# Kernel tuning notes

Hardware: AMD Instinct MI355X
Metric: run time of the kernel (lower is better)

The kernel has to match this reference:

```python
import jax, jax.numpy as jnp
import numpy as np

N, E = 50000, 800000
IN, HID, OUT = 128, 32, 8


def setup_inputs() -> dict:
    key = jax.random.key(0)
    ks = jax.random.split(key, 20)
    f32 = jnp.float32
    def rn(k, shape, s=0.1):
        return (jax.random.normal(k, shape, dtype=f32) * s)
    return {
        'x': jax.random.normal(ks[0], (N, IN), dtype=f32),
        'edge_index': jax.random.randint(ks[1], (2, E), 0, N, dtype=jnp.int32),
        'edge_attr': jax.random.uniform(ks[2], (E, 1), dtype=f32),
        # layer 1: heads=4, out=HID, concat -> 4*HID channels
        'w1l': rn(ks[3], (IN, 4 * HID)), 'b1l': rn(ks[4], (4 * HID,)),
        'w1r': rn(ks[5], (IN, 4 * HID)), 'b1r': rn(ks[6], (4 * HID,)),
        'w1e': rn(ks[7], (1, 4 * HID)),
        'att1': rn(ks[8], (4, HID)), 'bias1': rn(ks[9], (4 * HID,)),
        # layer 2: heads=2, out=HID, mean over heads -> HID channels
        'w2l': rn(ks[10], (4 * HID, 2 * HID)), 'b2l': rn(ks[11], (2 * HID,)),
        'w2r': rn(ks[12], (4 * HID, 2 * HID)), 'b2r': rn(ks[13], (2 * HID,)),
        'w2e': rn(ks[14], (1, 2 * HID)),
        'att2': rn(ks[15], (2, HID)), 'bias2': rn(ks[16], (HID,)),
        'wc': rn(ks[17], (HID, OUT)), 'bc': rn(ks[18], (OUT,)),
    }


def _add_self_loops(edge_index, edge_attr, n):
    # PyG GATv2Conv adds self-loops; edge feature for loops = mean of edge_attr
    loop = jnp.arange(n, dtype=edge_index.dtype)
    src = jnp.concatenate([edge_index[0], loop])
    dst = jnp.concatenate([edge_index[1], loop])
    mean_attr = jnp.broadcast_to(edge_attr.mean(axis=0), (n, edge_attr.shape[1]))
    ea = jnp.concatenate([edge_attr, mean_attr], axis=0)
    return src, dst, ea


def _gatv2(x, src, dst, eattr, Wl, bl, Wr, br, We, att, bias, heads, out, concat):
    n = x.shape[0]
    xl = (x @ Wl + bl).reshape(n, heads, out)   # source transform (messages)
    xr = (x @ Wr + br).reshape(n, heads, out)   # target transform
    e = (eattr @ We).reshape(-1, heads, out)    # edge embedding
    z = jax.nn.leaky_relu(xl[src] + xr[dst] + e, negative_slope=0.2)  # [Etot,H,D]
    score = jnp.einsum('ehd,hd->eh', z, att)
    # segment softmax over incoming edges of each destination node
    smax = jax.ops.segment_max(score, dst, num_segments=n)
    ex = jnp.exp(score - smax[dst])
    denom = jax.ops.segment_sum(ex, dst, num_segments=n)
    alpha = ex / denom[dst]                     # [Etot,H]
    agg = jax.ops.segment_sum(xl[src] * alpha[..., None], dst, num_segments=n)
    o = agg.reshape(n, heads * out) if concat else agg.mean(axis=1)
    return o + bias


def reference(x, edge_index, edge_attr, w1l, b1l, w1r, b1r, w1e, att1, bias1,
              w2l, b2l, w2r, b2r, w2e, att2, bias2, wc, bc):
    src, dst, ea = _add_self_loops(edge_index, edge_attr, x.shape[0])
    h = _gatv2(x, src, dst, ea, w1l, b1l, w1r, b1r, w1e, att1, bias1, 4, HID, True)
    h = jax.nn.elu(h)
    # dropout p=0.4 is training-only; reference is eval mode (identity)
    h = _gatv2(h, src, dst, ea, w2l, b2l, w2r, b2r, w2e, att2, bias2, 2, HID, False)
    h = jax.nn.elu(h)
    return h @ wc + bc
```

## Files before the change

kernel.cpp:

```cpp
#include <hip/hip_runtime.h>
#include <hip/hip_fp16.h>
#include <math.h>

typedef _Float16 h2_t __attribute__((ext_vector_type(2)));
typedef _Float16 h4_t __attribute__((ext_vector_type(4)));
typedef _Float16 h8_t __attribute__((ext_vector_type(8)));
typedef float f4_t __attribute__((ext_vector_type(4)));
typedef float f8_t __attribute__((ext_vector_type(8)));

#define PRE_BLOCKS 512

__device__ inline h8_t load8f_to_h8(const float* p) {
    float4 a = *(const float4*)p;
    float4 b = *(const float4*)(p + 4);
    h8_t r;
    r[0] = (_Float16)a.x; r[1] = (_Float16)a.y; r[2] = (_Float16)a.z; r[3] = (_Float16)a.w;
    r[4] = (_Float16)b.x; r[5] = (_Float16)b.y; r[6] = (_Float16)b.z; r[7] = (_Float16)b.w;
    return r;
}

__device__ inline h4_t load4f_to_h4(const float* p) {
    float4 a = *(const float4*)p;
    h4_t r;
    r[0] = (_Float16)a.x; r[1] = (_Float16)a.y; r[2] = (_Float16)a.z; r[3] = (_Float16)a.w;
    return r;
}

__device__ inline float dot8h(h8_t a, h8_t b, float s) {
    s = __builtin_amdgcn_fdot2(__builtin_shufflevector(a, a, 0, 1),
                               __builtin_shufflevector(b, b, 0, 1), s, false);
    s = __builtin_amdgcn_fdot2(__builtin_shufflevector(a, a, 2, 3),
                               __builtin_shufflevector(b, b, 2, 3), s, false);
    s = __builtin_amdgcn_fdot2(__builtin_shufflevector(a, a, 4, 5),
                               __builtin_shufflevector(b, b, 4, 5), s, false);
    s = __builtin_amdgcn_fdot2(__builtin_shufflevector(a, a, 6, 7),
                               __builtin_shufflevector(b, b, 6, 7), s, false);
    return s;
}

__device__ inline float dot4h(h4_t a, h4_t b, float s) {
    s = __builtin_amdgcn_fdot2(__builtin_shufflevector(a, a, 0, 1),
                               __builtin_shufflevector(b, b, 0, 1), s, false);
    s = __builtin_amdgcn_fdot2(__builtin_shufflevector(a, a, 2, 3),
                               __builtin_shufflevector(b, b, 2, 3), s, false);
    return s;
}

__device__ inline float elu1(float v) { return v > 0.f ? v : __expf(v) - 1.f; }

struct MA {
    const float* x;
    const float* eattr;
    const int* ei;
    const float *w1l, *b1l, *w1r, *b1r, *w1e, *att1, *bias1;
    const float *w2l, *b2l, *w2r, *b2r, *w2e, *att2, *bias2;
    const float *wc, *bc;
    float* out;
    _Float16 *xh, *xl1h, *xr1h, *h1h, *xl2h, *xr2h;
    _Float16 *p1l, *p1r, *p2l, *p2r;
    int *cnt, *offb, *rank;
    unsigned* flags;
    float* part;
    unsigned* edges;
    int N, E, NBs, NW;
    float invE;
};


__device__ inline void phase_packw(const MA& a, int g) {
    const float* W;
    _Float16* P;
    int M, lg;
    if (g < 2048)      { W = a.w1l; P = a.p1l; M = 128; lg = g; }
    else if (g < 4096) { W = a.w1r; P = a.p1r; M = 128; lg = g - 2048; }
    else if (g < 5120) { W = a.w2l; P = a.p2l; M = 64;  lg = g - 4096; }
    else               { W = a.w2r; P = a.p2r; M = 64;  lg = g - 5120; }
    int ln = lg & 63;
    int s = (lg >> 6) & 3;
    int tt = lg >> 8;
    int m = ln & 15, quad = ln >> 4;
    h8_t v;
#pragma unroll
    for (int j = 0; j < 8; ++j)
        v[j] = (_Float16)W[(size_t)(s * 32 + quad * 8 + j) * M + tt * 16 + m];
    *(h8_t*)(P + (size_t)lg * 8) = v;
}

template <int NT>
__device__ inline void phase_mm_tile(const MA& a, const _Float16* X, int rt, int lane,
                                     const _Float16* Pl, const float* bl, _Float16* Yl,
                                     const _Float16* Pr, const float* br, _Float16* Yr) {
    int nrow = lane & 15, quad = lane >> 4;
    int row = rt * 16 + nrow;
    if (row >= a.N) return;
    const _Float16* xp = X + (size_t)row * 128 + quad * 8;
    h8_t bf0 = *(const h8_t*)(xp);
    h8_t bf1 = *(const h8_t*)(xp + 32);
    h8_t bf2 = *(const h8_t*)(xp + 64);
    h8_t bf3 = *(const h8_t*)(xp + 96);
#pragma unroll
    for (int w = 0; w < 2; ++w) {
        const _Float16* P = w ? Pr : Pl;
        const float* bias = w ? br : bl;
        _Float16* Y = w ? Yr : Yl;
#pragma unroll
        for (int t2 = 0; t2 < NT; ++t2) {
            f4_t acc = {0.f, 0.f, 0.f, 0.f};
            const _Float16* pb = P + (size_t)t2 * 2048 + (size_t)lane * 8;
            acc = __builtin_amdgcn_mfma_f32_16x16x32_f16(*(const h8_t*)pb, bf0, acc, 0, 0, 0);
            acc = __builtin_amdgcn_mfma_f32_16x16x32_f16(*(const h8_t*)(pb + 512), bf1, acc, 0, 0, 0);
            acc = __builtin_amdgcn_mfma_f32_16x16x32_f16(*(const h8_t*)(pb + 1024), bf2, acc, 0, 0, 0);
            acc = __builtin_amdgcn_mfma_f32_16x16x32_f16(*(const h8_t*)(pb + 1536), bf3, acc, 0, 0, 0);
            float4 bv = *(const float4*)(bias + t2 * 16 + quad * 4);
            h4_t o;
            o[0] = (_Float16)(acc[0] + bv.x);
            o[1] = (_Float16)(acc[1] + bv.y);
            o[2] = (_Float16)(acc[2] + bv.z);
            o[3] = (_Float16)(acc[3] + bv.w);
            *(h4_t*)(Y + (size_t)row * (NT * 16) + t2 * 16 + quad * 4) = o;
        }
    }
}


__global__ __launch_bounds__(256) void k_pre(MA a) {
    if (blockIdx.x >= PRE_BLOCKS) {
        int g = (blockIdx.x - PRE_BLOCKS) * 256 + threadIdx.x;
        if (g < 6144) phase_packw(a, g);
        return;
    }
    int t = blockIdx.x * 256 + threadIdx.x;
    const int stride = PRE_BLOCKS * 256;
    for (int i = t; i < a.N; i += stride) a.cnt[i] = 0;
    for (int i = t; i < a.NBs; i += stride) a.flags[i] = 0u;
    int nchunk = (a.N * 128) >> 3;
    for (int i = t; i < nchunk; i += stride) {
        h8_t v = load8f_to_h8(a.x + (size_t)i * 8);
        *(h8_t*)(a.xh + (size_t)i * 8) = v;
    }
    float s = 0.f;
    for (int i = t; i < a.E; i += stride) s += a.eattr[i];
    __shared__ float sd[4];
    for (int o = 1; o < 64; o <<= 1) s += __shfl_xor(s, o, 64);
    if ((threadIdx.x & 63) == 0) sd[threadIdx.x >> 6] = s;
    __syncthreads();
    if (threadIdx.x == 0) a.part[blockIdx.x] = sd[0] + sd[1] + sd[2] + sd[3];
}


#define CNT_BLOCKS 1600

__global__ __launch_bounds__(256) void k_mmcnt(MA a) {
    int bid = blockIdx.x;
    if (bid < a.NW) {
        int wid = bid * 4 + (threadIdx.x >> 6);
        int ntile = (a.N + 15) / 16;
        if (wid < ntile)
            phase_mm_tile<8>(a, a.xh, wid, threadIdx.x & 63,
                             a.p1l, a.b1l, a.xl1h, a.p1r, a.b1r, a.xr1h);
    } else {
        int t = (bid - a.NW) * 256 + threadIdx.x;
        const int stride = CNT_BLOCKS * 256;
        for (int e = t; e < a.E; e += stride)
            a.rank[e] = atomicAdd(&a.cnt[a.ei[a.E + e]], 1);
    }
}


__global__ __launch_bounds__(256, 1) void k_scan(MA a) {
    __shared__ int tmp[256];
    __shared__ int sbase;
    __shared__ float smean;
    int tx = threadIdx.x;
    int b = blockIdx.x;
    int i = b * 256 + tx;
    {
        float s = a.part[tx] + a.part[tx + 256];
        for (int o = 1; o < 64; o <<= 1) s += __shfl_xor(s, o, 64);
        __shared__ float sd[4];
        if ((tx & 63) == 0) sd[tx >> 6] = s;
        __syncthreads();
        if (tx == 0) smean = (sd[0] + sd[1] + sd[2] + sd[3]) * a.invE;
    }
    int v = (i < a.N) ? a.cnt[i] + 1 : 0;
    tmp[tx] = v;
    __syncthreads();
    for (int o = 1; o < 256; o <<= 1) {
        int tv = (tx >= o) ? tmp[tx - o] : 0;
        __syncthreads();
        tmp[tx] += tv;
        __syncthreads();
    }
    int T = tmp[255];
    if (tx == 0) {
        if (b == 0) {
            atomicExch(&a.flags[0], (2u << 30) | (unsigned)T);
            sbase = 0;
        } else {
            atomicExch(&a.flags[b], (1u << 30) | (unsigned)T);
            int running = 0;
            int j = b - 1;
            while (true) {
                unsigned f = atomicAdd(&a.flags[j], 0u);
                unsigned st = f >> 30;
                if (st == 0u) continue;
                running += (int)(f & 0x3FFFFFFFu);
                if (st == 2u) break;
                --j;
            }
            atomicExch(&a.flags[b], (2u << 30) | (unsigned)(running + T));
            sbase = running;
        }
    }
    __syncthreads();
    if (i < a.N) {
        int o = sbase + tmp[tx] - v;
        a.offb[i] = o;
        unsigned qv = (unsigned)__float2int_rn(smean * 255.f);
        a.edges[o] = (unsigned)i | (qv << 24);
    }
}


__global__ __launch_bounds__(256) void k_fill(MA a) {
    int e = blockIdx.x * 256 + threadIdx.x;
    if (e >= a.E) return;
    int d = a.ei[a.E + e];
    int pos = a.offb[d] + 1 + a.rank[e];
    unsigned qv = (unsigned)__float2int_rn(a.eattr[e] * 255.f);
    a.edges[pos] = (unsigned)a.ei[e] | (qv << 24);
}


__global__ __launch_bounds__(256) void k_node1(MA a) {
    int lane = threadIdx.x & 63;
    int node = blockIdx.x * 4 + (threadIdx.x >> 6);
    if (node >= a.N) return;
    int g = lane >> 4;
    int q = lane & 15;
    int c0 = q * 8;

    h8_t xrv = *(const h8_t*)(a.xr1h + (size_t)node * 128 + c0);
    h8_t wev = load8f_to_h8(a.w1e + c0);
    h8_t atv = load8f_to_h8(a.att1 + c0);
    int start = a.offb[node];
    int deg1 = a.cnt[node] + 1;
    int last = deg1 - 1;

    float l = 0.f;
    f8_t acc = {0.f, 0.f, 0.f, 0.f, 0.f, 0.f, 0.f, 0.f};
    for (int i = 0; i < deg1; i += 16) {
        int s0 = i + g, s1 = i + 4 + g, s2 = i + 8 + g, s3 = i + 12 + g;
        unsigned p0 = a.edges[start + min(s0, last)];
        unsigned p1 = a.edges[start + min(s1, last)];
        unsigned p2 = a.edges[start + min(s2, last)];
        unsigned p3 = a.edges[start + min(s3, last)];
        h8_t x0 = *(const h8_t*)(a.xl1h + (size_t)(p0 & 0x00FFFFFFu) * 128 + c0);
        h8_t x1 = *(const h8_t*)(a.xl1h + (size_t)(p1 & 0x00FFFFFFu) * 128 + c0);
        h8_t x2 = *(const h8_t*)(a.xl1h + (size_t)(p2 & 0x00FFFFFFu) * 128 + c0);
        h8_t x3 = *(const h8_t*)(a.xl1h + (size_t)(p3 & 0x00FFFFFFu) * 128 + c0);
        float e0 = (float)(p0 >> 24) * (1.f / 255.f);
        float e1 = (float)(p1 >> 24) * (1.f / 255.f);
        float e2 = (float)(p2 >> 24) * (1.f / 255.f);
        float e3 = (float)(p3 >> 24) * (1.f / 255.f);
        h8_t z0 = x0 + xrv + wev * (_Float16)e0;
        z0 = __builtin_elementwise_max(z0, z0 * (_Float16)0.2f);
        float sc0 = dot8h(z0, atv, 0.f);
        h8_t z1 = x1 + xrv + wev * (_Float16)e1;
        z1 = __builtin_elementwise_max(z1, z1 * (_Float16)0.2f);
        float sc1 = dot8h(z1, atv, 0.f);
        h8_t z2 = x2 + xrv + wev * (_Float16)e2;
        z2 = __builtin_elementwise_max(z2, z2 * (_Float16)0.2f);
        float sc2 = dot8h(z2, atv, 0.f);
        h8_t z3 = x3 + xrv + wev * (_Float16)e3;
        z3 = __builtin_elementwise_max(z3, z3 * (_Float16)0.2f);
        float sc3 = dot8h(z3, atv, 0.f);
        sc0 += __shfl_xor(sc0, 1, 64); sc0 += __shfl_xor(sc0, 2, 64);
        sc1 += __shfl_xor(sc1, 1, 64); sc1 += __shfl_xor(sc1, 2, 64);
        sc2 += __shfl_xor(sc2, 1, 64); sc2 += __shfl_xor(sc2, 2, 64);
        sc3 += __shfl_xor(sc3, 1, 64); sc3 += __shfl_xor(sc3, 2, 64);
        float pA = (s0 < deg1) ? __expf(fminf(sc0, 60.f)) : 0.f;
        float pB = (s1 < deg1) ? __expf(fminf(sc1, 60.f)) : 0.f;
        float pC = (s2 < deg1) ? __expf(fminf(sc2, 60.f)) : 0.f;
        float pD = (s3 < deg1) ? __expf(fminf(sc3, 60.f)) : 0.f;
        l += (pA + pB) + (pC + pD);
#pragma unroll
        for (int k = 0; k < 8; ++k)
            acc[k] = fmaf(pA, (float)x0[k],
                     fmaf(pB, (float)x1[k],
                     fmaf(pC, (float)x2[k], fmaf(pD, (float)x3[k], acc[k]))));
    }
#pragma unroll
    for (int k = 0; k < 8; ++k) {
        acc[k] += __shfl_xor(acc[k], 16, 64);
        acc[k] += __shfl_xor(acc[k], 32, 64);
    }
    l += __shfl_xor(l, 16, 64);
    l += __shfl_xor(l, 32, 64);
    if (g == 0) {
        float inv = 1.f / l;
        float4 b0 = *(const float4*)(a.bias1 + c0);
        float4 b1 = *(const float4*)(a.bias1 + c0 + 4);
        float bb[8] = {b0.x, b0.y, b0.z, b0.w, b1.x, b1.y, b1.z, b1.w};
        h8_t o;
#pragma unroll
        for (int k = 0; k < 8; ++k) o[k] = (_Float16)elu1(fmaf(acc[k], inv, bb[k]));
        *(h8_t*)(a.h1h + (size_t)node * 128 + c0) = o;
    }
}


__global__ __launch_bounds__(256) void k_mm4(MA a) {
    int wid = blockIdx.x * 4 + (threadIdx.x >> 6);
    int ntile = (a.N + 15) / 16;
    if (wid >= ntile) return;
    phase_mm_tile<4>(a, a.h1h, wid, threadIdx.x & 63,
                     a.p2l, a.b2l, a.xl2h, a.p2r, a.b2r, a.xr2h);
}


__global__ __launch_bounds__(256) void k_node2(MA a) {
    __shared__ float h2s[16][33];
    int tid = threadIdx.x;
    int lane = tid & 63;
    int wib = tid >> 6;
    int sub = lane >> 4;
    int r = lane & 15;
    int nloc = wib * 4 + sub;
    int node = blockIdx.x * 16 + nloc;
    int c0 = r * 4;

    if (node < a.N) {
        h4_t xrv = *(const h4_t*)(a.xr2h + (size_t)node * 64 + c0);
        h4_t wev = load4f_to_h4(a.w2e + c0);
        h4_t atv = load4f_to_h4(a.att2 + c0);
        int start = a.offb[node];
        int deg1 = a.cnt[node] + 1;
        int last = deg1 - 1;
        float l = 0.f;
        float acc[4] = {0.f, 0.f, 0.f, 0.f};
        for (int i = 0; i < deg1; i += 4) {
            unsigned p[4];
            h4_t xv[4];
#pragma unroll
            for (int j = 0; j < 4; ++j) p[j] = a.edges[start + min(i + j, last)];
#pragma unroll
            for (int j = 0; j < 4; ++j)
                xv[j] = *(const h4_t*)(a.xl2h + (size_t)(p[j] & 0x00FFFFFFu) * 64 + c0);
#pragma unroll
            for (int j = 0; j < 4; ++j) {
                float ea = (float)(p[j] >> 24) * (1.f / 255.f);
                h4_t z = xv[j] + xrv + wev * (_Float16)ea;
                z = __builtin_elementwise_max(z, z * (_Float16)0.2f);
                float sc = dot4h(z, atv, 0.f);
                sc += __shfl_xor(sc, 1, 64);
                sc += __shfl_xor(sc, 2, 64);
                sc += __shfl_xor(sc, 4, 64);
                float pp = (i + j < deg1) ? __expf(fminf(sc, 60.f)) : 0.f;
                l += pp;
#pragma unroll
                for (int k = 0; k < 4; ++k) acc[k] = fmaf(pp, (float)xv[j][k], acc[k]);
            }
        }
        float inv = 1.f / l;
#pragma unroll
        for (int k = 0; k < 4; ++k) {
            float norm = acc[k] * inv;
            float other = __shfl_xor(norm, 8, 64);
            float v = 0.5f * (norm + other);
            if (r < 8) h2s[nloc][c0 + k] = elu1(v + a.bias2[c0 + k]);
        }
    }
    __syncthreads();
    if (tid < 128) {
        int n = tid >> 3, j = tid & 7;
        int gnode = blockIdx.x * 16 + n;
        if (gnode < a.N) {
            float acc = a.bc[j];
#pragma unroll 8
            for (int d = 0; d < 32; ++d) acc = fmaf(h2s[n][d], a.wc[d * 8 + j], acc);
            a.out[(size_t)gnode * 8 + j] = acc;
        }
    }
}


extern "C" void kernel_launch(void* const* d_in, const int* in_sizes, int n_in,
                              void* d_out, int out_size, void* d_ws, size_t ws_size,
                              hipStream_t stream) {
    const int N = in_sizes[0] / 128;
    const int E = in_sizes[2];
    const int tot = E + N;

    char* ws = (char*)d_ws;
    size_t o = 0;
    auto alloc = [&](size_t bytes) -> void* {
        void* p = ws + o;
        o += (bytes + 255) & ~(size_t)255;
        return p;
    };
    MA a;
    a.x     = (const float*)d_in[0];
    a.ei    = (const int*)d_in[1];
    a.eattr = (const float*)d_in[2];
    a.w1l = (const float*)d_in[3];  a.b1l = (const float*)d_in[4];
    a.w1r = (const float*)d_in[5];  a.b1r = (const float*)d_in[6];
    a.w1e = (const float*)d_in[7];  a.att1 = (const float*)d_in[8];
    a.bias1 = (const float*)d_in[9];
    a.w2l = (const float*)d_in[10]; a.b2l = (const float*)d_in[11];
    a.w2r = (const float*)d_in[12]; a.b2r = (const float*)d_in[13];
    a.w2e = (const float*)d_in[14]; a.att2 = (const float*)d_in[15];
    a.bias2 = (const float*)d_in[16];
    a.wc = (const float*)d_in[17];  a.bc = (const float*)d_in[18];
    a.out = (float*)d_out;

    a.xh   = (_Float16*)alloc((size_t)N * 128 * 2);
    a.xl1h = (_Float16*)alloc((size_t)N * 128 * 2);
    a.xr1h = (_Float16*)alloc((size_t)N * 128 * 2);
    a.h1h  = (_Float16*)alloc((size_t)N * 128 * 2);
    a.xl2h = (_Float16*)alloc((size_t)N * 64 * 2);
    a.xr2h = (_Float16*)alloc((size_t)N * 64 * 2);
    a.p1l  = (_Float16*)alloc(128 * 128 * 2);
    a.p1r  = (_Float16*)alloc(128 * 128 * 2);
    a.p2l  = (_Float16*)alloc(128 * 64 * 2);
    a.p2r  = (_Float16*)alloc(128 * 64 * 2);
    a.cnt  = (int*)alloc((size_t)N * 4);
    a.offb = (int*)alloc((size_t)N * 4);
    a.rank = (int*)alloc((size_t)E * 4);
    a.flags = (unsigned*)alloc(1024 * 4);
    a.part  = (float*)alloc(PRE_BLOCKS * 4);
    a.edges = (unsigned*)alloc((size_t)tot * 4);
    a.N = N;
    a.E = E;
    a.NBs = (N + 255) / 256;
    a.NW = (N + 63) / 64;
    a.invE = 1.0f / (float)E;

    k_pre<<<PRE_BLOCKS + 24, 256, 0, stream>>>(a);
    k_mmcnt<<<a.NW + CNT_BLOCKS, 256, 0, stream>>>(a);
    k_scan<<<a.NBs, 256, 0, stream>>>(a);
    k_fill<<<(E + 255) / 256, 256, 0, stream>>>(a);
    k_node1<<<(N + 3) / 4, 256, 0, stream>>>(a);
    k_mm4<<<(N + 63) / 64, 256, 0, stream>>>(a);
    k_node2<<<(N + 15) / 16, 256, 0, stream>>>(a);
}
```

Baseline: 279.4 us.

## Replace global atomic CSR build with two-level bucketed counting sort

Builds the destination-sorted edge list by radix-style bucketing: per-block LDS histograms over 64-node buckets, a column scan with decoupled lookback, LDS-atomic scatter into a temporary 64-bit buffer, then a per-bucket fine sort that computes offsets and degrees. This replaces per-edge global atomics on node counters and the separate rank array and fill pass. The aim is to remove contended global atomics and random scattered writes. In exchange it adds an extra pass over an 8-byte-per-edge temp buffer and a serial lookback scan.

```diff
diff --git a/kernel.cpp b/kernel.cpp
--- a/kernel.cpp
+++ b/kernel.cpp
@@ -9,6 +9,8 @@
 typedef float f8_t __attribute__((ext_vector_type(8)));
 
 #define PRE_BLOCKS 512
+#define SB 512
+#define NBUK_PAD 800
 
 __device__ inline h8_t load8f_to_h8(const float* p) {
     float4 a = *(const float4*)p;
@@ -58,11 +60,15 @@
     float* out;
     _Float16 *xh, *xl1h, *xr1h, *h1h, *xl2h, *xr2h;
     _Float16 *p1l, *p1r, *p2l, *p2r;
-    int *cnt, *offb, *rank;
+    int *deg, *offb;
+    unsigned* parth;
+    unsigned *tstart, *tot;
+    unsigned* smeanq;
+    unsigned long long* tmp;
     unsigned* flags;
     float* part;
     unsigned* edges;
-    int N, E, NBs, NW;
+    int N, E, NW, NBK, CE;
     float invE;
 };
 
@@ -129,10 +135,14 @@
         if (g < 6144) phase_packw(a, g);
         return;
     }
-    int t = blockIdx.x * 256 + threadIdx.x;
+    __shared__ unsigned bh[NBUK_PAD];
+    __shared__ float sd[4];
+    int tx = threadIdx.x;
+    for (int j = tx; j < NBUK_PAD; j += 256) bh[j] = 0u;
+
+    int t = blockIdx.x * 256 + tx;
     const int stride = PRE_BLOCKS * 256;
-    for (int i = t; i < a.N; i += stride) a.cnt[i] = 0;
-    for (int i = t; i < a.NBs; i += stride) a.flags[i] = 0u;
+    for (int i = t; i < NBUK_PAD; i += stride) a.flags[i] = 0u;
     int nchunk = (a.N * 128) >> 3;
     for (int i = t; i < nchunk; i += stride) {
         h8_t v = load8f_to_h8(a.x + (size_t)i * 8);
@@ -140,17 +150,77 @@
     }
     float s = 0.f;
     for (int i = t; i < a.E; i += stride) s += a.eattr[i];
-    __shared__ float sd[4];
     for (int o = 1; o < 64; o <<= 1) s += __shfl_xor(s, o, 64);
-    if ((threadIdx.x & 63) == 0) sd[threadIdx.x >> 6] = s;
-    __syncthreads();
-    if (threadIdx.x == 0) a.part[blockIdx.x] = sd[0] + sd[1] + sd[2] + sd[3];
-}
-
-
-#define CNT_BLOCKS 1600
-
-__global__ __launch_bounds__(256) void k_mmcnt(MA a) {
+    if ((tx & 63) == 0) sd[tx >> 6] = s;
+    __syncthreads();
+    if (tx == 0) a.part[blockIdx.x] = sd[0] + sd[1] + sd[2] + sd[3];
+
+    int e0 = blockIdx.x * a.CE, e1 = min(e0 + a.CE, a.E);
+    for (int e = e0 + tx; e < e1; e += 256)
+        atomicAdd(&bh[((unsigned)a.ei[a.E + e]) >> 6], 1u);
+    __syncthreads();
+    for (int j = tx; j < NBUK_PAD; j += 256)
+        a.parth[(size_t)blockIdx.x * NBUK_PAD + j] = bh[j];
+}
+
+
+__global__ __launch_bounds__(512, 1) void k_colscan(MA a) {
+    __shared__ unsigned lds[512];
+    __shared__ unsigned sbase;
+    __shared__ float sd[8];
+    int tx = threadIdx.x;
+    int b = blockIdx.x;
+    unsigned v = a.parth[(size_t)tx * NBUK_PAD + b];
+    lds[tx] = v;
+    __syncthreads();
+    for (int o = 1; o < 512; o <<= 1) {
+        unsigned u = (tx >= o) ? lds[tx - o] : 0u;
+        __syncthreads();
+        lds[tx] += u;
+        __syncthreads();
+    }
+    unsigned T = lds[511];
+    unsigned excl = lds[tx] - v;
+    if (tx == 0) {
+        unsigned run = 0;
+        if (b == 0) {
+            atomicExch(&a.flags[0], (2u << 30) | T);
+        } else {
+            atomicExch(&a.flags[b], (1u << 30) | T);
+            int j = b - 1;
+            while (true) {
+                unsigned f = atomicAdd(&a.flags[j], 0u);
+                unsigned st = f >> 30;
+                if (st == 0u) continue;
+                run += f & 0x3FFFFFFFu;
+                if (st == 2u) break;
+                --j;
+            }
+            atomicExch(&a.flags[b], (2u << 30) | (run + T));
+        }
+        a.tstart[b] = run;
+        a.tot[b] = T;
+        sbase = run;
+    }
+    __syncthreads();
+    a.parth[(size_t)tx * NBUK_PAD + b] = sbase + excl;
+
+    if (b == 0) {
+        float s = a.part[tx];
+        for (int o = 1; o < 64; o <<= 1) s += __shfl_xor(s, o, 64);
+        if ((tx & 63) == 0) sd[tx >> 6] = s;
+        __syncthreads();
+        if (tx == 0) {
+            float m = 0.f;
+#pragma unroll
+            for (int k = 0; k < 8; ++k) m += sd[k];
+            a.smeanq[0] = (unsigned)__float2int_rn(m * a.invE * 255.f);
+        }
+    }
+}
+
+
+__global__ __launch_bounds__(256) void k_scatter(MA a) {
     int bid = blockIdx.x;
     if (bid < a.NW) {
         int wid = bid * 4 + (threadIdx.x >> 6);
@@ -158,77 +228,66 @@
         if (wid < ntile)
             phase_mm_tile<8>(a, a.xh, wid, threadIdx.x & 63,
                              a.p1l, a.b1l, a.xl1h, a.p1r, a.b1r, a.xr1h);
-    } else {
-        int t = (bid - a.NW) * 256 + threadIdx.x;
-        const int stride = CNT_BLOCKS * 256;
-        for (int e = t; e < a.E; e += stride)
-            a.rank[e] = atomicAdd(&a.cnt[a.ei[a.E + e]], 1);
-    }
-}
-
-
-__global__ __launch_bounds__(256, 1) void k_scan(MA a) {
-    __shared__ int tmp[256];
-    __shared__ int sbase;
-    __shared__ float smean;
+        return;
+    }
+    __shared__ unsigned cur[NBUK_PAD];
+    int s = bid - a.NW;
     int tx = threadIdx.x;
+    for (int j = tx; j < NBUK_PAD; j += 256)
+        cur[j] = a.parth[(size_t)s * NBUK_PAD + j];
+    __syncthreads();
+    int e0 = s * a.CE, e1 = min(e0 + a.CE, a.E);
+    for (int e = e0 + tx; e < e1; e += 256) {
+        int d = a.ei[a.E + e];
+        unsigned src = (unsigned)a.ei[e];
+        unsigned q = (unsigned)__float2int_rn(a.eattr[e] * 255.f);
+        unsigned pos = atomicAdd(&cur[d >> 6], 1u);
+        a.tmp[pos] = ((unsigned long long)(unsigned)(d & 63) << 32) |
+                     (unsigned long long)(src | (q << 24));
+    }
+}
+
+
+__global__ __launch_bounds__(256) void k_fine(MA a) {
+    __shared__ int hist[64];
+    __shared__ unsigned cur[64];
+    __shared__ unsigned sm;
     int b = blockIdx.x;
-    int i = b * 256 + tx;
-    {
-        float s = a.part[tx] + a.part[tx + 256];
-        for (int o = 1; o < 64; o <<= 1) s += __shfl_xor(s, o, 64);
-        __shared__ float sd[4];
-        if ((tx & 63) == 0) sd[tx >> 6] = s;
-        __syncthreads();
-        if (tx == 0) smean = (sd[0] + sd[1] + sd[2] + sd[3]) * a.invE;
-    }
-    int v = (i < a.N) ? a.cnt[i] + 1 : 0;
-    tmp[tx] = v;
-    __syncthreads();
-    for (int o = 1; o < 256; o <<= 1) {
-        int tv = (tx >= o) ? tmp[tx - o] : 0;
-        __syncthreads();
-        tmp[tx] += tv;
-        __syncthreads();
-    }
-    int T = tmp[255];
-    if (tx == 0) {
-        if (b == 0) {
-            atomicExch(&a.flags[0], (2u << 30) | (unsigned)T);
-            sbase = 0;
-        } else {
-            atomicExch(&a.flags[b], (1u << 30) | (unsigned)T);
-            int running = 0;
-            int j = b - 1;
-            while (true) {
-                unsigned f = atomicAdd(&a.flags[j], 0u);
-                unsigned st = f >> 30;
-                if (st == 0u) continue;
-                running += (int)(f & 0x3FFFFFFFu);
-                if (st == 2u) break;
-                --j;
-            }
-            atomicExch(&a.flags[b], (2u << 30) | (unsigned)(running + T));
-            sbase = running;
-        }
-    }
-    __syncthreads();
-    if (i < a.N) {
-        int o = sbase + tmp[tx] - v;
-        a.offb[i] = o;
-        unsigned qv = (unsigned)__float2int_rn(smean * 255.f);
-        a.edges[o] = (unsigned)i | (qv << 24);
-    }
-}
-
-
-__global__ __launch_bounds__(256) void k_fill(MA a) {
-    int e = blockIdx.x * 256 + threadIdx.x;
-    if (e >= a.E) return;
-    int d = a.ei[a.E + e];
-    int pos = a.offb[d] + 1 + a.rank[e];
-    unsigned qv = (unsigned)__float2int_rn(a.eattr[e] * 255.f);
-    a.edges[pos] = (unsigned)a.ei[e] | (qv << 24);
+    int tx = threadIdx.x;
+    int n0 = b << 6;
+    int nn = min(64, a.N - n0);
+    unsigned ts = a.tstart[b], T = a.tot[b];
+    if (tx < 64) hist[tx] = 0;
+    if (tx == 0) sm = a.smeanq[0];
+    __syncthreads();
+    for (unsigned i = tx; i < T; i += 256) {
+        unsigned long long v = a.tmp[ts + i];
+        atomicAdd(&hist[(int)((v >> 32) & 63)], 1);
+    }
+    __syncthreads();
+    if (tx < 64) {
+        int deg1 = hist[tx] + 1;
+        int vsc = deg1;
+#pragma unroll
+        for (int o = 1; o < 64; o <<= 1) {
+            int u = __shfl_up(vsc, o, 64);
+            if (tx >= o) vsc += u;
+        }
+        int off = (int)ts + n0 + (vsc - deg1);
+        if (tx < nn) {
+            a.offb[n0 + tx] = off;
+            a.deg[n0 + tx] = deg1;
+            a.edges[off] = (unsigned)(n0 + tx) | (sm << 24);
+        }
+        cur[tx] = (unsigned)(off + 1);
+    }
+    __syncthreads();
+    for (unsigned i = tx; i < T; i += 256) {
+        unsigned long long v = a.tmp[ts + i];
+        int loc = (int)((v >> 32) & 63);
+        unsigned pos = atomicAdd(&cur[loc], 1u);
+        a.edges[pos] = (unsigned)v;
+    }
 }
 
 
@@ -244,7 +303,7 @@
     h8_t wev = load8f_to_h8(a.w1e + c0);
     h8_t atv = load8f_to_h8(a.att1 + c0);
     int start = a.offb[node];
-    int deg1 = a.cnt[node] + 1;
+    int deg1 = a.deg[node];
     int last = deg1 - 1;
 
     float l = 0.f;
@@ -335,7 +394,7 @@
         h4_t wev = load4f_to_h4(a.w2e + c0);
         h4_t atv = load4f_to_h4(a.att2 + c0);
         int start = a.offb[node];
-        int deg1 = a.cnt[node] + 1;
+        int deg1 = a.deg[node];
         int last = deg1 - 1;
         float l = 0.f;
         float acc[4] = {0.f, 0.f, 0.f, 0.f};
@@ -424,22 +483,27 @@
     a.p1r  = (_Float16*)alloc(128 * 128 * 2);
     a.p2l  = (_Float16*)alloc(128 * 64 * 2);
     a.p2r  = (_Float16*)alloc(128 * 64 * 2);
-    a.cnt  = (int*)alloc((size_t)N * 4);
+    a.deg  = (int*)alloc((size_t)N * 4);
     a.offb = (int*)alloc((size_t)N * 4);
-    a.rank = (int*)alloc((size_t)E * 4);
-    a.flags = (unsigned*)alloc(1024 * 4);
-    a.part  = (float*)alloc(PRE_BLOCKS * 4);
-    a.edges = (unsigned*)alloc((size_t)tot * 4);
+    a.parth  = (unsigned*)alloc((size_t)SB * NBUK_PAD * 4);
+    a.tstart = (unsigned*)alloc(NBUK_PAD * 4);
+    a.tot    = (unsigned*)alloc(NBUK_PAD * 4);
+    a.smeanq = (unsigned*)alloc(256);
+    a.flags  = (unsigned*)alloc(1024 * 4);
+    a.part   = (float*)alloc(PRE_BLOCKS * 4);
+    a.tmp    = (unsigned long long*)alloc((size_t)E * 8);
+    a.edges  = (unsigned*)alloc((size_t)tot * 4);
     a.N = N;
     a.E = E;
-    a.NBs = (N + 255) / 256;
     a.NW = (N + 63) / 64;
+    a.NBK = (N + 63) >> 6;
+    a.CE = (E + SB - 1) / SB;
     a.invE = 1.0f / (float)E;
 
     k_pre<<<PRE_BLOCKS + 24, 256, 0, stream>>>(a);
-    k_mmcnt<<<a.NW + CNT_BLOCKS, 256, 0, stream>>>(a);
-    k_scan<<<a.NBs, 256, 0, stream>>>(a);
-    k_fill<<<(E + 255) / 256, 256, 0, stream>>>(a);
+    k_colscan<<<a.NBK, 512, 0, stream>>>(a);
+    k_scatter<<<a.NW + SB, 256, 0, stream>>>(a);
+    k_fine<<<a.NBK, 256, 0, stream>>>(a);
     k_node1<<<(N + 3) / 4, 256, 0, stream>>>(a);
     k_mm4<<<(N + 63) / 64, 256, 0, stream>>>(a);
     k_node2<<<(N + 15) / 16, 256, 0, stream>>>(a);
```

Result: faster. 262.0 us (-6.2%).
